# Kernel optimization log

Hardware: AMD Instinct MI355X
Metric: run time of the kernel (lower is better)

The kernel has to match this reference:

```python
import jax, jax.numpy as jnp
import numpy as np

K = 1024          # num_embeddings
D = 64            # embedding_dim
BETA = 0.25
B, H, W = 32, 32, 32


def setup_inputs() -> dict:
    key = jax.random.key(0)
    k1, k2 = jax.random.split(key)
    x = jax.random.normal(k1, (B, D, H, W), dtype=jnp.float32)
    # embedding.weight.data.uniform_(-1/K, 1/K)
    emb_w = jax.random.uniform(k2, (K, D), dtype=jnp.float32, minval=-1.0 / K, maxval=1.0 / K)
    return {"x": x, "emb_w": emb_w}


def reference(x, emb_w):
    # x: [B, D, H, W] -> [B, H, W, D]
    xl = jnp.transpose(x, (0, 2, 3, 1))
    latents_shape = xl.shape
    flat = xl.reshape(-1, D)                         # [N, D]
    dist = ((flat ** 2).sum(axis=1, keepdims=True)
            + (emb_w ** 2).sum(axis=1)[None, :]
            - 2.0 * flat @ emb_w.T)
    idx = jnp.argmin(dist, axis=1)                   # [N]
    encoded = jax.nn.one_hot(idx, K, dtype=flat.dtype)  # [N, K]
    # gather (same math as encoded @ emb_w, avoids NxK matmul)
    quantized = emb_w[idx].reshape(latents_shape)    # [B, H, W, D]

    commitment_loss = jnp.mean((jax.lax.stop_gradient(quantized) - xl) ** 2)
    emb_loss = jnp.mean((quantized - jax.lax.stop_gradient(xl)) ** 2)
    vq_loss = commitment_loss + BETA * emb_loss

    # straight-through estimator
    quantized_st = xl + jax.lax.stop_gradient(quantized - xl)

    mean_probs = encoded.mean(axis=0)                # [K]
    perplexity = jnp.exp(-jnp.sum(mean_probs * jnp.log(mean_probs + 1e-10)))

    out = jnp.transpose(quantized_st, (0, 3, 1, 2))  # [B, D, H, W]
    return (out, vq_loss, perplexity, encoded)
```

## Files before the change

### kernel.cpp

```cpp
#include <hip/hip_runtime.h>

#define OUT_OFF_Q 0
#define OUT_OFF_VQ 2097152
#define OUT_OFF_PPL 2097153
#define OUT_OFF_ENC 2097154

typedef __attribute__((ext_vector_type(8))) short short8;
typedef __attribute__((ext_vector_type(4))) float f32x4;

__device__ __forceinline__ unsigned short f2bf(float f) {
    unsigned u = __builtin_bit_cast(unsigned, f);
    u += 0x7fffu + ((u >> 16) & 1u);
    return (unsigned short)(u >> 16);
}
__device__ __forceinline__ float bf2f(unsigned short h) {
    unsigned u = ((unsigned)h) << 16;
    return __builtin_bit_cast(float, u);
}

__global__ __launch_bounds__(64) void vq_prep(
    const float* __restrict__ E, unsigned short* __restrict__ Efrag,
    float* __restrict__ ee, int* __restrict__ counts)
{
    const int t = threadIdx.x;
    const int kt = blockIdx.x;
    const int code = kt * 16 + (t & 15);
    const int q = t >> 4;

    const float* ep0 = E + code * 64 + q * 8;
    const float* ep1 = ep0 + 32;
    short8 ah0, ah1, al0, al1;
    float s = 0.f;
    #pragma unroll
    for (int j = 0; j < 8; ++j) {
        float v0 = ep0[j];
        unsigned short h0 = f2bf(v0);
        ah0[j] = (short)h0;
        al0[j] = (short)f2bf(v0 - bf2f(h0));
        s = fmaf(v0, v0, s);
        float v1 = ep1[j];
        unsigned short h1 = f2bf(v1);
        ah1[j] = (short)h1;
        al1[j] = (short)f2bf(v1 - bf2f(h1));
        s = fmaf(v1, v1, s);
    }
    short8* dst = (short8*)Efrag + (size_t)kt * 256;
    dst[0 * 64 + t] = ah0;
    dst[1 * 64 + t] = ah1;
    dst[2 * 64 + t] = al0;
    dst[3 * 64 + t] = al1;

    s += __shfl_xor(s, 16);
    s += __shfl_xor(s, 32);
    if (t < 16) ee[code] = s;

    const int gid = blockIdx.x * 64 + t;
    if (gid < 1024) counts[gid] = 0;
}

__global__ __launch_bounds__(256, 4) void vq_main(
    const float* __restrict__ X, const float* __restrict__ E,
    const unsigned short* __restrict__ Efrag, const float* __restrict__ ee,
    float* __restrict__ out, int* __restrict__ counts,
    float* __restrict__ lossPart)
{
    __shared__ float s_ee[1024];
    __shared__ float s_val[4][32];
    __shared__ int   s_idx[4][32];
    __shared__ float s_loss[4];

    const int t = threadIdx.x;
    const int l = t & 63;
    const int w = __builtin_amdgcn_readfirstlane(t >> 6);
    const int col = l & 15;
    const int quad = l >> 4;
    const int n0 = blockIdx.x * 32;
    const int b = n0 >> 10;
    const int hwb = n0 & 1023;

    ((float4*)s_ee)[t] = ((const float4*)ee)[t];

    short8 bh[2][2], bl[2][2];
    const float* xb = X + (size_t)b * 65536 + hwb;
    #pragma unroll
    for (int nt = 0; nt < 2; ++nt) {
        const float* xn = xb + nt * 16 + col;
        #pragma unroll
        for (int ks = 0; ks < 2; ++ks) {
            short8 vh, vl;
            #pragma unroll
            for (int j = 0; j < 8; ++j) {
                float v = xn[(size_t)(ks * 32 + quad * 8 + j) * 1024];
                unsigned short hb = f2bf(v);
                vh[j] = (short)hb;
                vl[j] = (short)f2bf(v - bf2f(hb));
            }
            bh[nt][ks] = vh;
            bl[nt][ks] = vl;
        }
    }

    __syncthreads();

    float best[2] = {3.4e38f, 3.4e38f};
    int   bidx[2] = {0, 0};
    const short8* fw = (const short8*)Efrag + (size_t)(w * 16) * 256;
    #pragma unroll 2
    for (int kt = 0; kt < 16; ++kt) {
        const int kb = w * 256 + kt * 16;
        const short8* fb = fw + (size_t)kt * 256;
        short8 ah0 = fb[0 * 64 + l];
        short8 ah1 = fb[1 * 64 + l];
        short8 al0 = fb[2 * 64 + l];
        short8 al1 = fb[3 * 64 + l];
        f32x4 eev = *((const f32x4*)&s_ee[kb + quad * 4]);
        #pragma unroll
        for (int nt = 0; nt < 2; ++nt) {
            f32x4 c = {0.f, 0.f, 0.f, 0.f};
            c = __builtin_amdgcn_mfma_f32_16x16x32_bf16(ah0, bh[nt][0], c, 0, 0, 0);
            c = __builtin_amdgcn_mfma_f32_16x16x32_bf16(ah1, bh[nt][1], c, 0, 0, 0);
            c = __builtin_amdgcn_mfma_f32_16x16x32_bf16(al0, bh[nt][0], c, 0, 0, 0);
            c = __builtin_amdgcn_mfma_f32_16x16x32_bf16(al1, bh[nt][1], c, 0, 0, 0);
            c = __builtin_amdgcn_mfma_f32_16x16x32_bf16(ah0, bl[nt][0], c, 0, 0, 0);
            c = __builtin_amdgcn_mfma_f32_16x16x32_bf16(ah1, bl[nt][1], c, 0, 0, 0);
            #pragma unroll
            for (int r = 0; r < 4; ++r) {
                float val = fmaf(-2.f, c[r], eev[r]);
                int k = kb + quad * 4 + r;
                if (val < best[nt]) { best[nt] = val; bidx[nt] = k; }
            }
        }
    }

    #pragma unroll
    for (int nt = 0; nt < 2; ++nt) {
        float v = best[nt]; int i = bidx[nt];
        float ov = __shfl_xor(v, 16); int oi = __shfl_xor(i, 16);
        if (ov < v || (ov == v && oi < i)) { v = ov; i = oi; }
        ov = __shfl_xor(v, 32); oi = __shfl_xor(i, 32);
        if (ov < v || (ov == v && oi < i)) { v = ov; i = oi; }
        best[nt] = v; bidx[nt] = i;
    }
    if (quad < 2) {
        s_val[w][quad * 16 + col] = best[quad];
        s_idx[w][quad * 16 + col] = bidx[quad];
    }
    __syncthreads();

    if (t < 32) {
        float fv = s_val[0][t]; int fi0 = s_idx[0][t];
        #pragma unroll
        for (int j = 1; j < 4; ++j) {
            float v = s_val[j][t]; int i = s_idx[j][t];
            if (v < fv || (v == fv && i < fi0)) { fv = v; fi0 = i; }
        }
        s_idx[0][t] = fi0;
        atomicAdd(&counts[fi0], 1);
    }
    __syncthreads();

    {
        const int nl = l & 31;
        const int half = l >> 5;
        const int fi = s_idx[0][nl];
        const int hw = hwb + nl;
        const int d0 = (w << 4) + (half << 3);
        const float* er = E + ((size_t)fi << 6) + d0;
        float4 g0 = *(const float4*)(er);
        float4 g1 = *(const float4*)(er + 4);
        float q[8] = {g0.x, g0.y, g0.z, g0.w, g1.x, g1.y, g1.z, g1.w};
        float* op = out + OUT_OFF_Q + (size_t)b * 65536 + hw;
        const float* xp = X + (size_t)b * 65536 + hw;
        float lsum = 0.f;
        #pragma unroll
        for (int dd = 0; dd < 8; ++dd) {
            const int d = d0 + dd;
            op[(size_t)d * 1024] = q[dd];
            float diff = q[dd] - xp[(size_t)d * 1024];
            lsum = fmaf(diff, diff, lsum);
        }
        #pragma unroll
        for (int off = 32; off; off >>= 1) lsum += __shfl_down(lsum, off);
        if (l == 0) s_loss[w] = lsum;
    }
    __syncthreads();
    if (t == 0)
        lossPart[blockIdx.x] = s_loss[0] + s_loss[1] + s_loss[2] + s_loss[3];

    {
        f32x4* enc = (f32x4*)(out + OUT_OFF_ENC);
        const int rbase = w << 3;
        for (int rr = 0; rr < 8; ++rr) {
            const int r = rbase + rr;
            const int ridx = s_idx[0][r];
            f32x4* erow = enc + (size_t)(n0 + r) * 256;
            #pragma unroll
            for (int c4 = 0; c4 < 4; ++c4) {
                const int kb4 = (c4 << 8) + (l << 2);
                f32x4 v = {0.f, 0.f, 0.f, 0.f};
                const int dlt = ridx - kb4;
                if (dlt == 0) v.x = 1.f;
                else if (dlt == 1) v.y = 1.f;
                else if (dlt == 2) v.z = 1.f;
                else if (dlt == 3) v.w = 1.f;
                __builtin_nontemporal_store(v, erow + (c4 << 6) + l);
            }
        }
    }
}

__global__ __launch_bounds__(1024) void vq_finalize(
    const int* __restrict__ counts, const float* __restrict__ lossPart,
    float* __restrict__ out)
{
    __shared__ float redp[16];
    __shared__ float redl[16];
    const int t = threadIdx.x;
    const float p = (float)counts[t] * (1.0f / 32768.0f);
    float v = p * logf(p + 1e-10f);
    float ls = lossPart[t];
    #pragma unroll
    for (int off = 32; off; off >>= 1) {
        v += __shfl_down(v, off);
        ls += __shfl_down(ls, off);
    }
    if ((t & 63) == 0) { redp[t >> 6] = v; redl[t >> 6] = ls; }
    __syncthreads();
    if (t == 0) {
        float s = 0.f, sl = 0.f;
        #pragma unroll
        for (int i = 0; i < 16; ++i) { s += redp[i]; sl += redl[i]; }
        out[OUT_OFF_PPL] = expf(-s);
        out[OUT_OFF_VQ] = 1.25f * sl * (1.0f / 2097152.0f);
    }
}

extern "C" void kernel_launch(void* const* d_in, const int* in_sizes, int n_in,
                              void* d_out, int out_size, void* d_ws, size_t ws_size,
                              hipStream_t stream) {
    const float* X = (const float*)d_in[0];
    const float* E = (const float*)d_in[1];
    float* out = (float*)d_out;

    int* counts = (int*)d_ws;
    float* lossPart = (float*)((char*)d_ws + 4096);
    float* ee = (float*)((char*)d_ws + 8192);
    unsigned short* Efrag = (unsigned short*)((char*)d_ws + 12288);

    vq_prep<<<64, 64, 0, stream>>>(E, Efrag, ee, counts);
    vq_main<<<1024, 256, 0, stream>>>(X, E, Efrag, ee, out, counts, lossPart);
    vq_finalize<<<1, 1024, 0, stream>>>(counts, lossPart, out);
}
```

Measured before the change: 179.8 us.

## Double rows per block and fold finalize into main via last-block reduction

Each block now handles 64 rows instead of 32, so every codebook fragment loaded from global memory feeds twice as many MFMAs, and the grid shrinks to 512 blocks. Occupancy hint drops to 2 blocks per SM to leave room for the larger register footprint. The separate finalize kernel is removed; a done-counter atomic lets the last finishing block compute perplexity and loss, saving one launch at the cost of a threadfence and atomic per block.

```diff
diff --git a/kernel.cpp b/kernel.cpp
--- a/kernel.cpp
+++ b/kernel.cpp
@@ -20,7 +20,8 @@
 
 __global__ __launch_bounds__(64) void vq_prep(
     const float* __restrict__ E, unsigned short* __restrict__ Efrag,
-    float* __restrict__ ee, int* __restrict__ counts)
+    float* __restrict__ ee, int* __restrict__ counts,
+    unsigned int* __restrict__ doneCnt)
 {
     const int t = threadIdx.x;
     const int kt = blockIdx.x;
@@ -56,34 +57,36 @@
 
     const int gid = blockIdx.x * 64 + t;
     if (gid < 1024) counts[gid] = 0;
-}
-
-__global__ __launch_bounds__(256, 4) void vq_main(
+    if (gid == 1024) *doneCnt = 0u;
+}
+
+__global__ __launch_bounds__(256, 2) void vq_main(
     const float* __restrict__ X, const float* __restrict__ E,
     const unsigned short* __restrict__ Efrag, const float* __restrict__ ee,
     float* __restrict__ out, int* __restrict__ counts,
-    float* __restrict__ lossPart)
+    float* __restrict__ lossPart, unsigned int* __restrict__ doneCnt)
 {
     __shared__ float s_ee[1024];
-    __shared__ float s_val[4][32];
-    __shared__ int   s_idx[4][32];
+    __shared__ float s_val[4][64];
+    __shared__ int   s_idx[4][64];
     __shared__ float s_loss[4];
+    __shared__ int   s_last;
 
     const int t = threadIdx.x;
     const int l = t & 63;
     const int w = __builtin_amdgcn_readfirstlane(t >> 6);
     const int col = l & 15;
     const int quad = l >> 4;
-    const int n0 = blockIdx.x * 32;
+    const int n0 = blockIdx.x * 64;
     const int b = n0 >> 10;
     const int hwb = n0 & 1023;
 
     ((float4*)s_ee)[t] = ((const float4*)ee)[t];
 
-    short8 bh[2][2], bl[2][2];
+    short8 bh[4][2], bl[4][2];
     const float* xb = X + (size_t)b * 65536 + hwb;
     #pragma unroll
-    for (int nt = 0; nt < 2; ++nt) {
+    for (int nt = 0; nt < 4; ++nt) {
         const float* xn = xb + nt * 16 + col;
         #pragma unroll
         for (int ks = 0; ks < 2; ++ks) {
@@ -102,8 +105,8 @@
 
     __syncthreads();
 
-    float best[2] = {3.4e38f, 3.4e38f};
-    int   bidx[2] = {0, 0};
+    float best[4] = {3.4e38f, 3.4e38f, 3.4e38f, 3.4e38f};
+    int   bidx[4] = {0, 0, 0, 0};
     const short8* fw = (const short8*)Efrag + (size_t)(w * 16) * 256;
     #pragma unroll 2
     for (int kt = 0; kt < 16; ++kt) {
@@ -115,7 +118,7 @@
         short8 al1 = fb[3 * 64 + l];
         f32x4 eev = *((const f32x4*)&s_ee[kb + quad * 4]);
         #pragma unroll
-        for (int nt = 0; nt < 2; ++nt) {
+        for (int nt = 0; nt < 4; ++nt) {
             f32x4 c = {0.f, 0.f, 0.f, 0.f};
             c = __builtin_amdgcn_mfma_f32_16x16x32_bf16(ah0, bh[nt][0], c, 0, 0, 0);
             c = __builtin_amdgcn_mfma_f32_16x16x32_bf16(ah1, bh[nt][1], c, 0, 0, 0);
@@ -133,7 +136,7 @@
     }
 
     #pragma unroll
-    for (int nt = 0; nt < 2; ++nt) {
+    for (int nt = 0; nt < 4; ++nt) {
         float v = best[nt]; int i = bidx[nt];
         float ov = __shfl_xor(v, 16); int oi = __shfl_xor(i, 16);
         if (ov < v || (ov == v && oi < i)) { v = ov; i = oi; }
@@ -141,39 +144,38 @@
         if (ov < v || (ov == v && oi < i)) { v = ov; i = oi; }
         best[nt] = v; bidx[nt] = i;
     }
-    if (quad < 2) {
-        s_val[w][quad * 16 + col] = best[quad];
-        s_idx[w][quad * 16 + col] = bidx[quad];
-    }
-    __syncthreads();
-
-    if (t < 32) {
-        float fv = s_val[0][t]; int fi0 = s_idx[0][t];
+    s_val[w][quad * 16 + col] = best[quad];
+    s_idx[w][quad * 16 + col] = bidx[quad];
+    __syncthreads();
+
+    if (w == 0) {
+        float fv = s_val[0][l]; int fi0 = s_idx[0][l];
         #pragma unroll
         for (int j = 1; j < 4; ++j) {
-            float v = s_val[j][t]; int i = s_idx[j][t];
+            float v = s_val[j][l]; int i = s_idx[j][l];
             if (v < fv || (v == fv && i < fi0)) { fv = v; fi0 = i; }
         }
-        s_idx[0][t] = fi0;
+        s_idx[0][l] = fi0;
         atomicAdd(&counts[fi0], 1);
     }
     __syncthreads();
 
     {
-        const int nl = l & 31;
-        const int half = l >> 5;
-        const int fi = s_idx[0][nl];
-        const int hw = hwb + nl;
-        const int d0 = (w << 4) + (half << 3);
+        const int fi = s_idx[0][l];
+        const int hw = hwb + l;
+        const int d0 = w << 4;
         const float* er = E + ((size_t)fi << 6) + d0;
         float4 g0 = *(const float4*)(er);
         float4 g1 = *(const float4*)(er + 4);
-        float q[8] = {g0.x, g0.y, g0.z, g0.w, g1.x, g1.y, g1.z, g1.w};
+        float4 g2 = *(const float4*)(er + 8);
+        float4 g3 = *(const float4*)(er + 12);
+        float q[16] = {g0.x, g0.y, g0.z, g0.w, g1.x, g1.y, g1.z, g1.w,
+                       g2.x, g2.y, g2.z, g2.w, g3.x, g3.y, g3.z, g3.w};
         float* op = out + OUT_OFF_Q + (size_t)b * 65536 + hw;
         const float* xp = X + (size_t)b * 65536 + hw;
         float lsum = 0.f;
         #pragma unroll
-        for (int dd = 0; dd < 8; ++dd) {
+        for (int dd = 0; dd < 16; ++dd) {
             const int d = d0 + dd;
             op[(size_t)d * 1024] = q[dd];
             float diff = q[dd] - xp[(size_t)d * 1024];
@@ -189,8 +191,8 @@
 
     {
         f32x4* enc = (f32x4*)(out + OUT_OFF_ENC);
-        const int rbase = w << 3;
-        for (int rr = 0; rr < 8; ++rr) {
+        const int rbase = w << 4;
+        for (int rr = 0; rr < 16; ++rr) {
             const int r = rbase + rr;
             const int ridx = s_idx[0][r];
             f32x4* erow = enc + (size_t)(n0 + r) * 256;
@@ -207,31 +209,40 @@
             }
         }
     }
-}
-
-__global__ __launch_bounds__(1024) void vq_finalize(
-    const int* __restrict__ counts, const float* __restrict__ lossPart,
-    float* __restrict__ out)
-{
-    __shared__ float redp[16];
-    __shared__ float redl[16];
-    const int t = threadIdx.x;
-    const float p = (float)counts[t] * (1.0f / 32768.0f);
-    float v = p * logf(p + 1e-10f);
-    float ls = lossPart[t];
-    #pragma unroll
-    for (int off = 32; off; off >>= 1) {
-        v += __shfl_down(v, off);
-        ls += __shfl_down(ls, off);
-    }
-    if ((t & 63) == 0) { redp[t >> 6] = v; redl[t >> 6] = ls; }
+
+    __threadfence();
     __syncthreads();
     if (t == 0) {
-        float s = 0.f, sl = 0.f;
-        #pragma unroll
-        for (int i = 0; i < 16; ++i) { s += redp[i]; sl += redl[i]; }
-        out[OUT_OFF_PPL] = expf(-s);
-        out[OUT_OFF_VQ] = 1.25f * sl * (1.0f / 2097152.0f);
+        unsigned prev = __hip_atomic_fetch_add(doneCnt, 1u, __ATOMIC_ACQ_REL,
+                                               __HIP_MEMORY_SCOPE_AGENT);
+        s_last = (prev == 511u);
+    }
+    __syncthreads();
+    if (s_last) {
+        float pv = 0.f, lv = 0.f;
+        for (int i = t; i < 1024; i += 256) {
+            int c = __hip_atomic_load(&counts[i], __ATOMIC_RELAXED,
+                                      __HIP_MEMORY_SCOPE_AGENT);
+            float p = (float)c * (1.0f / 32768.0f);
+            pv += p * logf(p + 1e-10f);
+        }
+        for (int i = t; i < 512; i += 256) {
+            lv += __hip_atomic_load(&lossPart[i], __ATOMIC_RELAXED,
+                                    __HIP_MEMORY_SCOPE_AGENT);
+        }
+        #pragma unroll
+        for (int off = 32; off; off >>= 1) {
+            pv += __shfl_down(pv, off);
+            lv += __shfl_down(lv, off);
+        }
+        if (l == 0) { s_val[0][w] = pv; s_val[1][w] = lv; }
+        __syncthreads();
+        if (t == 0) {
+            float sp = s_val[0][0] + s_val[0][1] + s_val[0][2] + s_val[0][3];
+            float sl = s_val[1][0] + s_val[1][1] + s_val[1][2] + s_val[1][3];
+            out[OUT_OFF_PPL] = expf(-sp);
+            out[OUT_OFF_VQ] = 1.25f * sl * (1.0f / 2097152.0f);
+        }
     }
 }
 
@@ -243,11 +254,12 @@
     float* out = (float*)d_out;
 
     int* counts = (int*)d_ws;
-    float* lossPart = (float*)((char*)d_ws + 4096);
-    float* ee = (float*)((char*)d_ws + 8192);
-    unsigned short* Efrag = (unsigned short*)((char*)d_ws + 12288);
-
-    vq_prep<<<64, 64, 0, stream>>>(E, Efrag, ee, counts);
-    vq_main<<<1024, 256, 0, stream>>>(X, E, Efrag, ee, out, counts, lossPart);
-    vq_finalize<<<1, 1024, 0, stream>>>(counts, lossPart, out);
-}
+    unsigned int* doneCnt = (unsigned int*)((char*)d_ws + 4096);
+    float* lossPart = (float*)((char*)d_ws + 8192);
+    float* ee = (float*)((char*)d_ws + 12288);
+    unsigned short* Efrag = (unsigned short*)((char*)d_ws + 16384);
+
+    vq_prep<<<64, 64, 0, stream>>>(E, Efrag, ee, counts, doneCnt);
+    vq_main<<<512, 256, 0, stream>>>(X, E, Efrag, ee, out, counts,
+                                     lossPart, doneCnt);
+}
```

New measurement: 286.3 us. 59.2% more time.
